# Kernel optimization log

Measured on AMD Instinct MI355X. Metric: run time of the kernel, lower is better.

The kernel has to match this reference:

```python
import jax, jax.numpy as jnp
import numpy as np
from math import sqrt

MIN_WINDOW, MAX_WINDOW = 1.0, 10000.0


def rope_consecutive(x):
    # x: [B, S, H, D]; TE 'consecutive' rotary: pairs are adjacent (even, odd) lanes.
    d = x.shape[-1]
    half = d // 2
    fraction = 2.0 * jnp.arange(half, dtype=jnp.float32) / d
    time_scales = MIN_WINDOW * (MAX_WINDOW / MIN_WINDOW) ** fraction          # [D/2]
    time_scales = jnp.repeat(time_scales, 2)                                   # [D]
    positions = jnp.arange(x.shape[1], dtype=jnp.float32)                      # [S]
    sinusoid = positions[None, :, None, None] / time_scales                    # [1,S,1,D]
    sin, cos = jnp.sin(sinusoid), jnp.cos(sinusoid)
    idx = jnp.arange(d)
    odd = (idx % 2) == 1                                                       # [D]
    # even lanes take left neighbor (roll -1), odd lanes take right neighbor (roll +1)
    x_shifted = jnp.where(odd, jnp.roll(x, 1, axis=-1), jnp.roll(x, -1, axis=-1))
    sign = jnp.where(odd, 1.0, -1.0)
    return (x * cos + x_shifted * sin * sign).astype(x.dtype)


def setup_inputs() -> dict:
    key = jax.random.key(0)
    k1, k2, k3 = jax.random.split(key, 3)
    B, S, M, H, D = 4, 2048, 2048, 16, 128
    x = jax.random.normal(k1, (B, S, M), dtype=jnp.float32)
    Wqkv = jax.random.normal(k2, (M, 3, H, D), dtype=jnp.float32) / sqrt(M)
    Wo = jax.random.normal(k3, (H * D, M), dtype=jnp.float32) / sqrt(H * D)
    return {"x": x, "Wqkv": Wqkv, "Wo": Wo}


def reference(x, Wqkv, Wo):
    # x: [B,S,M]; Wqkv: [M,3,H,D]; Wo: [H*D,M]
    B, S, M = x.shape
    H, D = Wqkv.shape[2], Wqkv.shape[3]
    qkv = jnp.einsum('bsm,mthd->bsthd', x, Wqkv)  # packed BS3HD projection
    q, k, v = qkv[:, :, 0], qkv[:, :, 1], qkv[:, :, 2]  # each [B,S,H,D]
    q = rope_consecutive(q)
    k = rope_consecutive(k)
    scale = 1.0 / sqrt(D)
    scores = jnp.einsum('bqhd,bkhd->bhqk', q, k) * scale  # [B,H,S,S]
    causal = jnp.tril(jnp.ones((S, S), dtype=bool))
    scores = jnp.where(causal[None, None], scores, jnp.finfo(scores.dtype).min)
    probs = jax.nn.softmax(scores, axis=-1)
    ctx = jnp.einsum('bhqk,bkhd->bqhd', probs, v)  # [B,S,H,D]
    out = jnp.einsum('bqhd,xm->bqm', ctx, jnp.zeros((0, 0))) if False else ctx.reshape(B, S, H * D) @ Wo
    return out
```

## Files before the change

### kernel.cpp

```cpp
#include <hip/hip_runtime.h>
#include <hip/hip_bf16.h>

#define B_ 4
#define S_ 2048
#define M_ 2048
#define H_ 16
#define D_ 128
#define ROWS (B_*S_)
#define CQKV (3*H_*D_)

typedef __bf16 bf16x8 __attribute__((ext_vector_type(8)));
typedef float f32x4 __attribute__((ext_vector_type(4)));
typedef unsigned short u16x8 __attribute__((ext_vector_type(8)));
typedef unsigned short u16x4 __attribute__((ext_vector_type(4)));

__device__ __forceinline__ unsigned short f2bf(float x) {
    unsigned u = __builtin_bit_cast(unsigned, x);
    u += 0x7fffu + ((u >> 16) & 1u);
    return (unsigned short)(u >> 16);
}
__device__ __forceinline__ float bf2f(unsigned short u) {
    return __builtin_bit_cast(float, (unsigned)u << 16);
}

__device__ __forceinline__ void gld_lds16(const unsigned short* g, unsigned short* l) {
    __builtin_amdgcn_global_load_lds(
        (__attribute__((address_space(1))) void*)g,
        (__attribute__((address_space(3))) void*)l,
        16, 0, 0);
}


__global__ __launch_bounds__(256) void cvt_bf16(const float* __restrict__ in,
                                                unsigned short* __restrict__ out) {
    int idx = (blockIdx.x * 256 + threadIdx.x) * 4;
    float4 v = *(const float4*)&in[idx];
    u16x4 o = { f2bf(v.x), f2bf(v.y), f2bf(v.z), f2bf(v.w) };
    *(u16x4*)&out[idx] = o;
}

__global__ __launch_bounds__(256) void cvt_transpose(const float* __restrict__ in,
                                                     unsigned short* __restrict__ out,
                                                     int R, int C) {
    __shared__ unsigned short tile[32][33];
    int c0 = blockIdx.x * 32, r0 = blockIdx.y * 32;
    int tx = threadIdx.x, ty = threadIdx.y;
#pragma unroll
    for (int i = 0; i < 4; ++i)
        tile[ty + i * 8][tx] = f2bf(in[(size_t)(r0 + ty + i * 8) * C + c0 + tx]);
    __syncthreads();
#pragma unroll
    for (int i = 0; i < 4; ++i)
        out[(size_t)(c0 + ty + i * 8) * R + r0 + tx] = tile[tx][ty + i * 8];
}


#define BM2 256
#define BN2 256
#define BK2 64
#define NT2 (M_/BK2)

#define STAGE(p_, u_, mat_, h_) do {                                                     \
        const unsigned short* _s = (mat_) ? Bg : Ag;                                     \
        const size_t _r = (size_t)((((mat_) ? c0 : r0) + (h_) * 128) + w * 8 + srow) * M_ \
                          + (u_) * BK2 + scol;                                           \
        unsigned short* _l = &lds[(p_) * 32768 + (mat_) * 16384 + (h_) * 8192 + w * 512]; \
        gld_lds16(&_s[_r], _l);                                                          \
        gld_lds16(&_s[_r + (size_t)64 * M_], _l + 4096);                                 \
    } while (0)

#define BAR() asm volatile("s_barrier" ::: "memory")

#define GEMM_MAIN_LOOP()                                                                  \
    const int srow = lane >> 3;                                                           \
    const int scol = ((lane & 7) ^ srow) * 8;                                             \
    const int axor = lcol & 7;                                                            \
    const int k0off = (lq ^ axor) * 8;                                                    \
    const int k1off = ((4 | lq) ^ axor) * 8;                                              \
    const int arow = wr * 8192 + lcol * 64;                                               \
    const int brow = 16384 + (wc >> 1) * 8192 + ((wc & 1) * 64 + lcol) * 64;              \
    f32x4 acc[8][4];                                                                      \
    _Pragma("unroll") for (int i = 0; i < 8; ++i)                                         \
        _Pragma("unroll") for (int j = 0; j < 4; ++j) acc[i][j] = (f32x4){0.f,0.f,0.f,0.f};\
    STAGE(0, 0, 0, 0); STAGE(0, 0, 0, 1); STAGE(0, 0, 1, 0); STAGE(0, 0, 1, 1);           \
    STAGE(1, 1, 1, 0); STAGE(1, 1, 1, 1);                                                 \
    asm volatile("s_waitcnt vmcnt(4)" ::: "memory");                                      \
    BAR();                                                                                \
    bf16x8 a[4][2], b[4][2];                                                              \
    for (int t = 0; t < NT2; ++t) {                                                       \
        const int bo = (t & 1) * 32768;                                                   \
        const int pn = (t + 1) & 1;                                                       \
        const int u1 = (t + 1 < NT2) ? (t + 1) : (NT2 - 1);                               \
        const int u2 = (t + 2 < NT2) ? (t + 2) : (NT2 - 1);                               \
        _Pragma("unroll") for (int i = 0; i < 4; ++i) {                                   \
            a[i][0] = *(const bf16x8*)&lds[bo + arow + i * 1024 + k0off];                  \
            a[i][1] = *(const bf16x8*)&lds[bo + arow + i * 1024 + k1off];                  \
        }                                                                                 \
        _Pragma("unroll") for (int j = 0; j < 2; ++j) {                                   \
            b[j][0] = *(const bf16x8*)&lds[bo + brow + j * 1024 + k0off];                  \
            b[j][1] = *(const bf16x8*)&lds[bo + brow + j * 1024 + k1off];                  \
        }                                                                                 \
        STAGE(pn, u1, 0, 0);                                                              \
        BAR();                                                                            \
        __builtin_amdgcn_s_setprio(1);                                                    \
        _Pragma("unroll") for (int i = 0; i < 4; ++i)                                     \
            _Pragma("unroll") for (int j = 0; j < 2; ++j) {                               \
                acc[i][j] = __builtin_amdgcn_mfma_f32_16x16x32_bf16(a[i][0], b[j][0], acc[i][j], 0, 0, 0); \
                acc[i][j] = __builtin_amdgcn_mfma_f32_16x16x32_bf16(a[i][1], b[j][1], acc[i][j], 0, 0, 0); \
            }                                                                             \
        __builtin_amdgcn_s_setprio(0);                                                    \
        BAR();                                                                            \
        _Pragma("unroll") for (int j = 2; j < 4; ++j) {                                   \
            b[j][0] = *(const bf16x8*)&lds[bo + brow + j * 1024 + k0off];                  \
            b[j][1] = *(const bf16x8*)&lds[bo + brow + j * 1024 + k1off];                  \
        }                                                                                 \
        STAGE(pn, u1, 0, 1);                                                              \
        BAR();                                                                            \
        __builtin_amdgcn_s_setprio(1);                                                    \
        _Pragma("unroll") for (int i = 0; i < 4; ++i)                                     \
            _Pragma("unroll") for (int j = 2; j < 4; ++j) {                               \
                acc[i][j] = __builtin_amdgcn_mfma_f32_16x16x32_bf16(a[i][0], b[j][0], acc[i][j], 0, 0, 0); \
                acc[i][j] = __builtin_amdgcn_mfma_f32_16x16x32_bf16(a[i][1], b[j][1], acc[i][j], 0, 0, 0); \
            }                                                                             \
        __builtin_amdgcn_s_setprio(0);                                                    \
        BAR();                                                                            \
        _Pragma("unroll") for (int i = 0; i < 4; ++i) {                                   \
            a[i][0] = *(const bf16x8*)&lds[bo + arow + (i + 4) * 1024 + k0off];            \
            a[i][1] = *(const bf16x8*)&lds[bo + arow + (i + 4) * 1024 + k1off];            \
        }                                                                                 \
        STAGE(t & 1, u2, 1, 0);                                                           \
        BAR();                                                                            \
        __builtin_amdgcn_s_setprio(1);                                                    \
        _Pragma("unroll") for (int i = 0; i < 4; ++i)                                     \
            _Pragma("unroll") for (int j = 2; j < 4; ++j) {                               \
                acc[i + 4][j] = __builtin_amdgcn_mfma_f32_16x16x32_bf16(a[i][0], b[j][0], acc[i + 4][j], 0, 0, 0); \
                acc[i + 4][j] = __builtin_amdgcn_mfma_f32_16x16x32_bf16(a[i][1], b[j][1], acc[i + 4][j], 0, 0, 0); \
            }                                                                             \
        __builtin_amdgcn_s_setprio(0);                                                    \
        BAR();                                                                            \
        STAGE(t & 1, u2, 1, 1);                                                           \
        BAR();                                                                            \
        __builtin_amdgcn_s_setprio(1);                                                    \
        _Pragma("unroll") for (int i = 0; i < 4; ++i)                                     \
            _Pragma("unroll") for (int j = 0; j < 2; ++j) {                               \
                acc[i + 4][j] = __builtin_amdgcn_mfma_f32_16x16x32_bf16(a[i][0], b[j][0], acc[i + 4][j], 0, 0, 0); \
                acc[i + 4][j] = __builtin_amdgcn_mfma_f32_16x16x32_bf16(a[i][1], b[j][1], acc[i + 4][j], 0, 0, 0); \
            }                                                                             \
        __builtin_amdgcn_s_setprio(0);                                                    \
        asm volatile("s_waitcnt vmcnt(4)" ::: "memory");                                  \
        BAR();                                                                            \
    }


__global__ __launch_bounds__(512, 2) void gemm_qkv_rope(
    const unsigned short* __restrict__ xb,
    const unsigned short* __restrict__ wT,
    unsigned short* __restrict__ qg,
    unsigned short* __restrict__ kg,
    unsigned short* __restrict__ vt) {
    __shared__ unsigned short lds[65536];

    const int tid = threadIdx.x;
    const int lane = tid & 63;
    const int w = tid >> 6;
    const int wr = w >> 2;
    const int wc = w & 3;
    const int lcol = lane & 15;
    const int lq = lane >> 4;

    const int lin = (int)(blockIdx.y * gridDim.x + blockIdx.x);
    const int swz = (lin & 7) * 96 + (lin >> 3);
    const int r0 = (swz / 24) * BM2;
    const int c0 = (swz % 24) * BN2;

    const unsigned short* Ag = xb;
    const unsigned short* Bg = wT;

    GEMM_MAIN_LOOP()

    const int colbase = c0 + wc * 64;
    const int tix = colbase >> 11;
    const int hh = (colbase & 2047) >> 7;
    if (tix < 2) {
        unsigned short* dst = (tix == 0) ? qg : kg;
#pragma unroll
        for (int j = 0; j < 4; ++j) {
            const int d = (wc & 1) * 64 + j * 16 + lcol;
            float inv_ts = exp2f(-(float)(d >> 1) * (13.28771237954945f / 64.0f));
            float sw, cw;
            __sincosf(inv_ts, &sw, &cw);
#pragma unroll
            for (int i = 0; i < 8; ++i) {
                int row0 = r0 + wr * 128 + i * 16 + lq * 4;
                int bb = row0 >> 11, s0 = row0 & 2047;
                float sn, cs;
                __sincosf((float)s0 * inv_ts, &sn, &cs);
                size_t base = (size_t)((bb * H_ + hh) * S_ + s0) * D_ + d;
#pragma unroll
                for (int r = 0; r < 4; ++r) {
                    float val = acc[i][j][r];
                    float pr = __shfl_xor(val, 1);
                    float v2 = (d & 1) ? (val * cs + pr * sn) : (val * cs - pr * sn);
                    dst[base + (size_t)r * D_] = f2bf(v2);
                    float ns = sn * cw + cs * sw;
                    float nc = cs * cw - sn * sw;
                    sn = ns; cs = nc;
                }
            }
        }
    } else {
#pragma unroll
        for (int j = 0; j < 4; ++j) {
            const int d = (wc & 1) * 64 + j * 16 + lcol;
#pragma unroll
            for (int i = 0; i < 8; ++i) {
                int row0 = r0 + wr * 128 + i * 16 + lq * 4;
                int bb = row0 >> 11, s0 = row0 & 2047;
                u16x4 v4 = { f2bf(acc[i][j][0]), f2bf(acc[i][j][1]),
                             f2bf(acc[i][j][2]), f2bf(acc[i][j][3]) };
                *(u16x4*)&vt[(size_t)((bb * H_ + hh) * D_ + d) * S_ + s0] = v4;
            }
        }
    }
}


__global__ __launch_bounds__(512, 2) void gemm_out(
    const unsigned short* __restrict__ ctx,
    const unsigned short* __restrict__ woT,
    float* __restrict__ out) {
    __shared__ unsigned short lds[65536];

    const int tid = threadIdx.x;
    const int lane = tid & 63;
    const int w = tid >> 6;
    const int wr = w >> 2;
    const int wc = w & 3;
    const int lcol = lane & 15;
    const int lq = lane >> 4;

    const int lin = (int)(blockIdx.y * gridDim.x + blockIdx.x);
    const int swz = (lin & 7) * 32 + (lin >> 3);
    const int r0 = (swz >> 3) * BM2;
    const int c0 = (swz & 7) * BN2;

    const unsigned short* Ag = ctx;
    const unsigned short* Bg = woT;

    GEMM_MAIN_LOOP()

#pragma unroll
    for (int i = 0; i < 8; ++i) {
#pragma unroll
        for (int r = 0; r < 4; ++r) {
            int row = r0 + wr * 128 + i * 16 + lq * 4 + r;
#pragma unroll
            for (int j = 0; j < 4; ++j) {
                int col = c0 + wc * 64 + j * 16 + lcol;
                out[(size_t)row * M_ + col] = acc[i][j][r];
            }
        }
    }
}

#undef STAGE
#undef BAR


__global__ __launch_bounds__(256, 2) void attn(
    const unsigned short* __restrict__ qg,
    const unsigned short* __restrict__ kg,
    const unsigned short* __restrict__ vt,
    unsigned short* __restrict__ ctx) {
    __shared__ unsigned short Ks[64 * 136];
    __shared__ unsigned short VTs[128 * 72];
    __shared__ unsigned short Ps[128 * 72];

    const int tid = threadIdx.x, lane = tid & 63, wave = tid >> 6;

    const int lin = (int)(blockIdx.y * gridDim.x + blockIdx.x);
    const int idx = lin >> 3;
    const int bh = ((lin & 7) << 3) + (idx >> 4);
    const int q0 = (15 - (idx & 15)) * 128;
    const int q0w = q0 + wave * 32;
    const unsigned short* qb = qg + (size_t)bh * S_ * D_;
    const unsigned short* kb = kg + (size_t)bh * S_ * D_;
    const unsigned short* vtb = vt + (size_t)bh * S_ * D_;

    const int lcol = lane & 15;
    const int lq = lane >> 4;

    const float scale = 0.08838834764831845f;
    bf16x8 qf[2][4];
#pragma unroll
    for (int f = 0; f < 2; ++f)
#pragma unroll
        for (int kk = 0; kk < 4; ++kk) {
            u16x8 raw = *(const u16x8*)&qb[(size_t)(q0w + f * 16 + lcol) * D_ + kk * 32 + lq * 8];
            u16x8 sc8;
#pragma unroll
            for (int j = 0; j < 8; ++j) sc8[j] = f2bf(bf2f(raw[j]) * scale);
            qf[f][kk] = __builtin_bit_cast(bf16x8, sc8);
        }

    f32x4 o[2][8];
#pragma unroll
    for (int f = 0; f < 2; ++f)
#pragma unroll
        for (int ot = 0; ot < 8; ++ot) o[f][ot] = (f32x4){0.f, 0.f, 0.f, 0.f};
    float lsum[2][4] = {{0.f, 0.f, 0.f, 0.f}, {0.f, 0.f, 0.f, 0.f}};

    const int kv_last = q0 + 64;

    u16x8 kpre[4], vpre[4];
#pragma unroll
    for (int j = 0; j < 4; ++j) {
        int c = tid + j * 256;
        kpre[j] = *(const u16x8*)&kb[(size_t)(c >> 4) * D_ + (c & 15) * 8];
        vpre[j] = *(const u16x8*)&vtb[(size_t)(c >> 3) * S_ + (c & 7) * 8];
    }

    for (int kv0 = 0; kv0 <= kv_last; kv0 += 64) {
        __syncthreads();
#pragma unroll
        for (int j = 0; j < 4; ++j) {
            int c = tid + j * 256;
            *(u16x8*)&Ks[(c >> 4) * 136 + (c & 15) * 8] = kpre[j];
            *(u16x8*)&VTs[(c >> 3) * 72 + (c & 7) * 8] = vpre[j];
        }
        __syncthreads();
        if (kv0 + 64 <= kv_last) {
#pragma unroll
            for (int j = 0; j < 4; ++j) {
                int c = tid + j * 256;
                kpre[j] = *(const u16x8*)&kb[(size_t)(kv0 + 64 + (c >> 4)) * D_ + (c & 15) * 8];
                vpre[j] = *(const u16x8*)&vtb[(size_t)(c >> 3) * S_ + kv0 + 64 + (c & 7) * 8];
            }
        }

        if (kv0 <= q0w + 31) {
            f32x4 sc[2][4];
            __builtin_amdgcn_s_setprio(1);
#pragma unroll
            for (int nt = 0; nt < 4; ++nt) {
                f32x4 a0 = (f32x4){0.f, 0.f, 0.f, 0.f};
                f32x4 a1 = (f32x4){0.f, 0.f, 0.f, 0.f};
#pragma unroll
                for (int kk = 0; kk < 4; ++kk) {
                    bf16x8 kf = *(const bf16x8*)&Ks[(nt * 16 + lcol) * 136 + kk * 32 + lq * 8];
                    a0 = __builtin_amdgcn_mfma_f32_16x16x32_bf16(qf[0][kk], kf, a0, 0, 0, 0);
                    a1 = __builtin_amdgcn_mfma_f32_16x16x32_bf16(qf[1][kk], kf, a1, 0, 0, 0);
                }
                sc[0][nt] = a0; sc[1][nt] = a1;
            }
            __builtin_amdgcn_s_setprio(0);

#pragma unroll
            for (int f = 0; f < 2; ++f) {
                if (kv0 + 63 > q0w + f * 16) {
#pragma unroll
                    for (int nt = 0; nt < 4; ++nt)
#pragma unroll
                        for (int r = 0; r < 4; ++r) {
                            int skv = kv0 + nt * 16 + lcol;
                            int sq = q0w + f * 16 + lq * 4 + r;
                            float p = (skv > sq) ? 0.f : __expf(sc[f][nt][r]);
                            sc[f][nt][r] = p;
                            lsum[f][r] += p;
                        }
                } else {
#pragma unroll
                    for (int nt = 0; nt < 4; ++nt)
#pragma unroll
                        for (int r = 0; r < 4; ++r) {
                            float p = __expf(sc[f][nt][r]);
                            sc[f][nt][r] = p;
                            lsum[f][r] += p;
                        }
                }
#pragma unroll
                for (int nt = 0; nt < 4; ++nt)
#pragma unroll
                    for (int r = 0; r < 4; ++r)
                        Ps[(wave * 32 + f * 16 + lq * 4 + r) * 72 + nt * 16 + lcol] = f2bf(sc[f][nt][r]);
            }

            __builtin_amdgcn_s_setprio(1);
#pragma unroll
            for (int kk = 0; kk < 2; ++kk) {
                bf16x8 pf0 = *(const bf16x8*)&Ps[(wave * 32 + lcol) * 72 + kk * 32 + lq * 8];
                bf16x8 pf1 = *(const bf16x8*)&Ps[(wave * 32 + 16 + lcol) * 72 + kk * 32 + lq * 8];
#pragma unroll
                for (int ot = 0; ot < 8; ++ot) {
                    bf16x8 vf = *(const bf16x8*)&VTs[(ot * 16 + lcol) * 72 + kk * 32 + lq * 8];
                    o[0][ot] = __builtin_amdgcn_mfma_f32_16x16x32_bf16(pf0, vf, o[0][ot], 0, 0, 0);
                    o[1][ot] = __builtin_amdgcn_mfma_f32_16x16x32_bf16(pf1, vf, o[1][ot], 0, 0, 0);
                }
            }
            __builtin_amdgcn_s_setprio(0);
        }
    }

#pragma unroll
    for (int f = 0; f < 2; ++f)
#pragma unroll
        for (int r = 0; r < 4; ++r) {
#pragma unroll
            for (int off = 1; off < 16; off <<= 1) lsum[f][r] += __shfl_xor(lsum[f][r], off);
        }

    const int b = bh >> 4, h = bh & 15;
#pragma unroll
    for (int f = 0; f < 2; ++f)
#pragma unroll
        for (int r = 0; r < 4; ++r) {
            float invl = 1.0f / lsum[f][r];
            int s = q0w + f * 16 + lq * 4 + r;
#pragma unroll
            for (int ot = 0; ot < 8; ++ot) {
                int d = ot * 16 + lcol;
                ctx[(size_t)(b * S_ + s) * (H_ * D_) + h * D_ + d] = f2bf(o[f][ot][r] * invl);
            }
        }
}


extern "C" void kernel_launch(void* const* d_in, const int* in_sizes, int n_in,
                              void* d_out, int out_size, void* d_ws, size_t ws_size,
                              hipStream_t stream) {
    const float* x = (const float*)d_in[0];
    const float* Wqkv = (const float*)d_in[1];
    const float* Wo = (const float*)d_in[2];
    float* out = (float*)d_out;

    unsigned short* xb = (unsigned short*)d_ws;
    unsigned short* wT = xb + (size_t)ROWS * M_;
    unsigned short* woT = wT + (size_t)CQKV * M_;
    unsigned short* qg = woT + (size_t)M_ * M_;
    unsigned short* kg = qg + (size_t)B_ * H_ * S_ * D_;
    unsigned short* vtw = kg + (size_t)B_ * H_ * S_ * D_;
    unsigned short* ctxp = vtw + (size_t)B_ * H_ * S_ * D_;

    cvt_bf16<<<(ROWS * M_) / 1024, 256, 0, stream>>>(x, xb);
    cvt_transpose<<<dim3(CQKV / 32, M_ / 32), dim3(32, 8), 0, stream>>>(Wqkv, wT, M_, CQKV);
    cvt_transpose<<<dim3(M_ / 32, M_ / 32), dim3(32, 8), 0, stream>>>(Wo, woT, M_, M_);

    gemm_qkv_rope<<<dim3(CQKV / BN2, ROWS / BM2), 512, 0, stream>>>(xb, wT, qg, kg, vtw);
    attn<<<dim3(S_ / 128, B_ * H_), 256, 0, stream>>>(qg, kg, vtw, ctxp);
    gemm_out<<<dim3(M_ / BN2, ROWS / BM2), 512, 0, stream>>>(ctxp, woT, out);
}
```

Before: 566.1 us.

## Double-buffer K/V shared tiles and replace padding with XOR swizzle in attention

The attention kernel now keeps two shared-memory buffers for the K and V^T tiles. The next tile is stored into the idle buffer after the current tile's MFMAs, which cuts the loop from two block barriers per iteration to one. Row padding in the K, V^T and P tiles is replaced by XOR-swizzled 16-byte chunk indexing to avoid bank conflicts without padding. Shared memory use rises to about 80KB per block, which could limit occupancy at the requested two blocks per CU.

```diff
diff --git a/kernel.cpp b/kernel.cpp
--- a/kernel.cpp
+++ b/kernel.cpp
@@ -272,9 +272,9 @@
     const unsigned short* __restrict__ kg,
     const unsigned short* __restrict__ vt,
     unsigned short* __restrict__ ctx) {
-    __shared__ unsigned short Ks[64 * 136];
-    __shared__ unsigned short VTs[128 * 72];
-    __shared__ unsigned short Ps[128 * 72];
+    __shared__ unsigned short Ks[2][64 * 128];
+    __shared__ unsigned short VTs[2][128 * 64];
+    __shared__ unsigned short Ps[128 * 64];
 
     const int tid = threadIdx.x, lane = tid & 63, wave = tid >> 6;
 
@@ -319,17 +319,19 @@
         kpre[j] = *(const u16x8*)&kb[(size_t)(c >> 4) * D_ + (c & 15) * 8];
         vpre[j] = *(const u16x8*)&vtb[(size_t)(c >> 3) * S_ + (c & 7) * 8];
     }
+#pragma unroll
+    for (int j = 0; j < 4; ++j) {
+        int c = tid + j * 256;
+        *(u16x8*)&Ks[0][(c >> 4) * 128 + (((c & 15) ^ ((c >> 4) & 15)) * 8)] = kpre[j];
+        *(u16x8*)&VTs[0][(c >> 3) * 64 + (((c & 7) ^ ((c >> 3) & 7)) * 8)] = vpre[j];
+    }
+    __syncthreads();
 
     for (int kv0 = 0; kv0 <= kv_last; kv0 += 64) {
-        __syncthreads();
-#pragma unroll
-        for (int j = 0; j < 4; ++j) {
-            int c = tid + j * 256;
-            *(u16x8*)&Ks[(c >> 4) * 136 + (c & 15) * 8] = kpre[j];
-            *(u16x8*)&VTs[(c >> 3) * 72 + (c & 7) * 8] = vpre[j];
-        }
-        __syncthreads();
-        if (kv0 + 64 <= kv_last) {
+        const int cur = (kv0 >> 6) & 1;
+        const bool more = (kv0 + 64 <= kv_last);
+
+        if (more) {
 #pragma unroll
             for (int j = 0; j < 4; ++j) {
                 int c = tid + j * 256;
@@ -347,7 +349,7 @@
                 f32x4 a1 = (f32x4){0.f, 0.f, 0.f, 0.f};
 #pragma unroll
                 for (int kk = 0; kk < 4; ++kk) {
-                    bf16x8 kf = *(const bf16x8*)&Ks[(nt * 16 + lcol) * 136 + kk * 32 + lq * 8];
+                    bf16x8 kf = *(const bf16x8*)&Ks[cur][(nt * 16 + lcol) * 128 + (((kk * 4 + lq) ^ lcol) * 8)];
                     a0 = __builtin_amdgcn_mfma_f32_16x16x32_bf16(qf[0][kk], kf, a0, 0, 0, 0);
                     a1 = __builtin_amdgcn_mfma_f32_16x16x32_bf16(qf[1][kk], kf, a1, 0, 0, 0);
                 }
@@ -381,24 +383,38 @@
 #pragma unroll
                 for (int nt = 0; nt < 4; ++nt)
 #pragma unroll
-                    for (int r = 0; r < 4; ++r)
-                        Ps[(wave * 32 + f * 16 + lq * 4 + r) * 72 + nt * 16 + lcol] = f2bf(sc[f][nt][r]);
+                    for (int r = 0; r < 4; ++r) {
+                        int prow = wave * 32 + f * 16 + lq * 4 + r;
+                        int pch = (nt * 2 + (lcol >> 3)) ^ (prow & 7);
+                        Ps[prow * 64 + pch * 8 + (lcol & 7)] = f2bf(sc[f][nt][r]);
+                    }
             }
 
             __builtin_amdgcn_s_setprio(1);
 #pragma unroll
             for (int kk = 0; kk < 2; ++kk) {
-                bf16x8 pf0 = *(const bf16x8*)&Ps[(wave * 32 + lcol) * 72 + kk * 32 + lq * 8];
-                bf16x8 pf1 = *(const bf16x8*)&Ps[(wave * 32 + 16 + lcol) * 72 + kk * 32 + lq * 8];
+                int pxor = ((kk * 4 + lq) ^ (lcol & 7)) * 8;
+                bf16x8 pf0 = *(const bf16x8*)&Ps[(wave * 32 + lcol) * 64 + pxor];
+                bf16x8 pf1 = *(const bf16x8*)&Ps[(wave * 32 + 16 + lcol) * 64 + pxor];
 #pragma unroll
                 for (int ot = 0; ot < 8; ++ot) {
-                    bf16x8 vf = *(const bf16x8*)&VTs[(ot * 16 + lcol) * 72 + kk * 32 + lq * 8];
+                    bf16x8 vf = *(const bf16x8*)&VTs[cur][(ot * 16 + lcol) * 64 + pxor];
                     o[0][ot] = __builtin_amdgcn_mfma_f32_16x16x32_bf16(pf0, vf, o[0][ot], 0, 0, 0);
                     o[1][ot] = __builtin_amdgcn_mfma_f32_16x16x32_bf16(pf1, vf, o[1][ot], 0, 0, 0);
                 }
             }
             __builtin_amdgcn_s_setprio(0);
         }
+
+        if (more) {
+#pragma unroll
+            for (int j = 0; j < 4; ++j) {
+                int c = tid + j * 256;
+                *(u16x8*)&Ks[cur ^ 1][(c >> 4) * 128 + (((c & 15) ^ ((c >> 4) & 15)) * 8)] = kpre[j];
+                *(u16x8*)&VTs[cur ^ 1][(c >> 3) * 64 + (((c & 7) ^ ((c >> 3) & 7)) * 8)] = vpre[j];
+            }
+        }
+        __syncthreads();
     }
 
 #pragma unroll
```

Measured after the change: 588.0 us. 3.9% more time.

## Keep attention probabilities in registers by computing transposed scores

Applied to the files above, without the earlier changes.

Swaps the MFMA operands of the QK^T product so each lane holds scores along the key dimension, which lets the bf16 probabilities feed the PV MFMA directly as register operands. The shared-memory P buffer, along with its stores and reloads, is removed, and PV moves from 16x16x32 to 16x16x16 MFMAs. Row sums become a per-lane scalar that is reduced across lane groups and broadcast with a shuffle at the end. The trade is twice as many PV MFMA instructions and narrower VT loads from LDS, in exchange for no P round-trip through LDS and less shared memory, which may help occupancy.

```diff
diff --git a/kernel.cpp b/kernel.cpp
--- a/kernel.cpp
+++ b/kernel.cpp
@@ -13,6 +13,7 @@
 typedef float f32x4 __attribute__((ext_vector_type(4)));
 typedef unsigned short u16x8 __attribute__((ext_vector_type(8)));
 typedef unsigned short u16x4 __attribute__((ext_vector_type(4)));
+typedef short s16x4 __attribute__((ext_vector_type(4)));
 
 __device__ __forceinline__ unsigned short f2bf(float x) {
     unsigned u = __builtin_bit_cast(unsigned, x);
@@ -274,7 +275,6 @@
     unsigned short* __restrict__ ctx) {
     __shared__ unsigned short Ks[64 * 136];
     __shared__ unsigned short VTs[128 * 72];
-    __shared__ unsigned short Ps[128 * 72];
 
     const int tid = threadIdx.x, lane = tid & 63, wave = tid >> 6;
 
@@ -308,7 +308,7 @@
     for (int f = 0; f < 2; ++f)
 #pragma unroll
         for (int ot = 0; ot < 8; ++ot) o[f][ot] = (f32x4){0.f, 0.f, 0.f, 0.f};
-    float lsum[2][4] = {{0.f, 0.f, 0.f, 0.f}, {0.f, 0.f, 0.f, 0.f}};
+    float lsum[2] = {0.f, 0.f};
 
     const int kv_last = q0 + 64;
 
@@ -348,53 +348,53 @@
 #pragma unroll
                 for (int kk = 0; kk < 4; ++kk) {
                     bf16x8 kf = *(const bf16x8*)&Ks[(nt * 16 + lcol) * 136 + kk * 32 + lq * 8];
-                    a0 = __builtin_amdgcn_mfma_f32_16x16x32_bf16(qf[0][kk], kf, a0, 0, 0, 0);
-                    a1 = __builtin_amdgcn_mfma_f32_16x16x32_bf16(qf[1][kk], kf, a1, 0, 0, 0);
+                    a0 = __builtin_amdgcn_mfma_f32_16x16x32_bf16(kf, qf[0][kk], a0, 0, 0, 0);
+                    a1 = __builtin_amdgcn_mfma_f32_16x16x32_bf16(kf, qf[1][kk], a1, 0, 0, 0);
                 }
                 sc[0][nt] = a0; sc[1][nt] = a1;
             }
             __builtin_amdgcn_s_setprio(0);
 
+            s16x4 pa[2][4];
 #pragma unroll
             for (int f = 0; f < 2; ++f) {
-                if (kv0 + 63 > q0w + f * 16) {
-#pragma unroll
-                    for (int nt = 0; nt < 4; ++nt)
+                const int sq = q0w + f * 16 + lcol;
+                if (kv0 + 63 > sq) {
+#pragma unroll
+                    for (int nt = 0; nt < 4; ++nt) {
+                        u16x4 pk;
 #pragma unroll
                         for (int r = 0; r < 4; ++r) {
-                            int skv = kv0 + nt * 16 + lcol;
-                            int sq = q0w + f * 16 + lq * 4 + r;
+                            int skv = kv0 + nt * 16 + lq * 4 + r;
                             float p = (skv > sq) ? 0.f : __expf(sc[f][nt][r]);
-                            sc[f][nt][r] = p;
-                            lsum[f][r] += p;
+                            lsum[f] += p;
+                            pk[r] = f2bf(p);
                         }
+                        pa[f][nt] = __builtin_bit_cast(s16x4, pk);
+                    }
                 } else {
 #pragma unroll
-                    for (int nt = 0; nt < 4; ++nt)
+                    for (int nt = 0; nt < 4; ++nt) {
+                        u16x4 pk;
 #pragma unroll
                         for (int r = 0; r < 4; ++r) {
                             float p = __expf(sc[f][nt][r]);
-                            sc[f][nt][r] = p;
-                            lsum[f][r] += p;
+                            lsum[f] += p;
+                            pk[r] = f2bf(p);
                         }
+                        pa[f][nt] = __builtin_bit_cast(s16x4, pk);
+                    }
                 }
-#pragma unroll
-                for (int nt = 0; nt < 4; ++nt)
-#pragma unroll
-                    for (int r = 0; r < 4; ++r)
-                        Ps[(wave * 32 + f * 16 + lq * 4 + r) * 72 + nt * 16 + lcol] = f2bf(sc[f][nt][r]);
             }
 
             __builtin_amdgcn_s_setprio(1);
 #pragma unroll
-            for (int kk = 0; kk < 2; ++kk) {
-                bf16x8 pf0 = *(const bf16x8*)&Ps[(wave * 32 + lcol) * 72 + kk * 32 + lq * 8];
-                bf16x8 pf1 = *(const bf16x8*)&Ps[(wave * 32 + 16 + lcol) * 72 + kk * 32 + lq * 8];
+            for (int nt = 0; nt < 4; ++nt) {
 #pragma unroll
                 for (int ot = 0; ot < 8; ++ot) {
-                    bf16x8 vf = *(const bf16x8*)&VTs[(ot * 16 + lcol) * 72 + kk * 32 + lq * 8];
-                    o[0][ot] = __builtin_amdgcn_mfma_f32_16x16x32_bf16(pf0, vf, o[0][ot], 0, 0, 0);
-                    o[1][ot] = __builtin_amdgcn_mfma_f32_16x16x32_bf16(pf1, vf, o[1][ot], 0, 0, 0);
+                    s16x4 vf = *(const s16x4*)&VTs[(ot * 16 + lcol) * 72 + nt * 16 + lq * 4];
+                    o[0][ot] = __builtin_amdgcn_mfma_f32_16x16x16bf16_1k(pa[0][nt], vf, o[0][ot], 0, 0, 0);
+                    o[1][ot] = __builtin_amdgcn_mfma_f32_16x16x16bf16_1k(pa[1][nt], vf, o[1][ot], 0, 0, 0);
                 }
             }
             __builtin_amdgcn_s_setprio(0);
@@ -402,19 +402,18 @@
     }
 
 #pragma unroll
+    for (int f = 0; f < 2; ++f) {
+        lsum[f] += __shfl_xor(lsum[f], 16);
+        lsum[f] += __shfl_xor(lsum[f], 32);
+    }
+
+    const int b = bh >> 4, h = bh & 15;
+#pragma unroll
     for (int f = 0; f < 2; ++f)
 #pragma unroll
         for (int r = 0; r < 4; ++r) {
-#pragma unroll
-            for (int off = 1; off < 16; off <<= 1) lsum[f][r] += __shfl_xor(lsum[f][r], off);
-        }
-
-    const int b = bh >> 4, h = bh & 15;
-#pragma unroll
-    for (int f = 0; f < 2; ++f)
-#pragma unroll
-        for (int r = 0; r < 4; ++r) {
-            float invl = 1.0f / lsum[f][r];
+            float lv = __shfl(lsum[f], lq * 4 + r);
+            float invl = 1.0f / lv;
             int s = q0w + f * 16 + lq * 4 + r;
 #pragma unroll
             for (int ot = 0; ot < 8; ++ot) {
```

Result: no change. 555.6 us (-1.9%).
